# Optimization experiments

Measured on AMD Instinct MI355X. Metric: run time of the kernel, lower is better.

## Reference

```python
import jax, jax.numpy as jnp
import numpy as np

SPP_SIZES = (1, 3, 6, 8)  # -> 1+9+36+64 = 110 pooled tokens


def conv1x1(x, w, b):
    # x: [B,C,H,W], w: [O,C], b: [O] -> [B,O,H,W]
    return jnp.einsum('bchw,oc->bohw', x, w) + b[None, :, None, None]


def spp(t):
    # t: [B,C,H,W] with H,W divisible by every size -> [B,C,110]
    B, C, H, W = t.shape
    outs = []
    for s in SPP_SIZES:
        p = t.reshape(B, C, s, H // s, s, W // s).mean(axis=(3, 5))
        outs.append(p.reshape(B, C, s * s))
    return jnp.concatenate(outs, axis=-1)


def setup_inputs() -> dict:
    key = jax.random.key(0)
    ks = jax.random.split(key, 9)
    B, C, H, W = 8, 512, 96, 96
    inner = 256
    sc = 1.0 / np.sqrt(C)
    return {
        'x': jax.random.normal(ks[0], (B, C, H, W), dtype=jnp.float32),
        'phi_w': jax.random.normal(ks[1], (inner, C), dtype=jnp.float32) * sc,
        'phi_b': jnp.zeros((inner,), dtype=jnp.float32),
        'theta_w': jax.random.normal(ks[2], (inner, C), dtype=jnp.float32) * sc,
        'theta_b': jnp.zeros((inner,), dtype=jnp.float32),
        'gamma_w': jax.random.normal(ks[3], (inner, C), dtype=jnp.float32) * sc,
        'gamma_b': jnp.zeros((inner,), dtype=jnp.float32),
        'W_w': jax.random.normal(ks[4], (C, inner), dtype=jnp.float32) * (1.0 / np.sqrt(inner)),
        'W_b': jnp.zeros((C,), dtype=jnp.float32),
    }


def reference(x, phi_w, phi_b, theta_w, theta_b, gamma_w, gamma_b, W_w, W_b):
    B, C, H, W = x.shape
    HW = H * W
    phi = jax.nn.relu(conv1x1(x, phi_w, phi_b))      # [B,256,H,W]
    theta = jax.nn.relu(conv1x1(x, theta_w, theta_b))
    gamma = conv1x1(x, gamma_w, gamma_b)
    theta_p = spp(theta)                              # [B,256,110]
    gamma_p = spp(gamma)                              # [B,256,110]
    # Faithful to original: raw reshape (NOT a transpose) of [B,256,H,W] -> [B,HW,256]
    phi_r = jnp.reshape(phi, (B, HW, 256))
    y1 = jnp.einsum('bnc,bck->bnk', phi_r, theta_p)   # [B,HW,110]
    y1_norm = jax.nn.softmax(y1 * (HW ** -0.25), axis=-1)
    y2 = jnp.einsum('bnk,bkc->bnc', y1_norm, jnp.transpose(gamma_p, (0, 2, 1)))  # [B,HW,256]
    # Faithful raw reshape back to [B,256,H,W]
    y2_r = jnp.reshape(y2, (B, 256, H, W))
    y2_w = conv1x1(y2_r, W_w, W_b)                    # [B,C,H,W]
    return x + y2_w
```

## Files before the change

### kernel.cpp

```cpp
#include <hip/hip_runtime.h>

#define NB 8
#define CIN 512
#define OIN 256
#define HWN 9216
#define KP 110
#define SCL 0.10206207261596577f

typedef __attribute__((ext_vector_type(8))) short bf16x8;
typedef __attribute__((ext_vector_type(4))) float f32x4;
typedef unsigned short u16;

__device__ inline unsigned bf16_1(float a) {
    unsigned u = __builtin_bit_cast(unsigned, a);
    return (u + 0x7fffu + ((u >> 16) & 1u)) >> 16;
}
__device__ inline unsigned bf16_pack(float a, float b) {
    return bf16_1(a) | (bf16_1(b) << 16);
}
__device__ inline float b2f(u16 u) {
    return __builtin_bit_cast(float, ((unsigned)u) << 16);
}

__device__ __forceinline__ void gload16(const u16* g, u16* l) {
    __builtin_amdgcn_global_load_lds(
        (const __attribute__((address_space(1))) unsigned int*)g,
        (__attribute__((address_space(3))) unsigned int*)l, 16, 0, 0);
}

__global__ __launch_bounds__(256) void castw_kernel(
    const float* __restrict__ phi_w, const float* __restrict__ theta_w,
    const float* __restrict__ Ww,
    u16* __restrict__ Wcat, u16* __restrict__ Wwb)
{
    int i = blockIdx.x * 256 + threadIdx.x;
    if (i < 262144) {
        float v = (i < 131072) ? phi_w[i] : theta_w[i - 131072];
        Wcat[i] = (u16)bf16_1(v);
    } else {
        int j = i - 262144;
        Wwb[j] = (u16)bf16_1(Ww[j]);
    }
}

__global__ __launch_bounds__(256) void castx_kernel(
    const float* __restrict__ x, u16* __restrict__ xT)
{
    const int t = threadIdx.x;
    const int tx = t & 15, ty = t >> 4;
    const int b = blockIdx.z;
    const int c0 = blockIdx.y * 64;
    const int hw0 = blockIdx.x * 64;

    const float* xb = x + ((size_t)b * CIN + c0 + ty * 4) * HWN + hw0 + tx * 4;
    float4 v[4];
#pragma unroll
    for (int q = 0; q < 4; ++q)
        v[q] = *(const float4*)(xb + (size_t)q * HWN);

    u16* dst = xT + ((size_t)b * HWN + hw0 + tx * 4) * CIN + c0 + ty * 4;
    const float* f = (const float*)v;
#pragma unroll
    for (int p = 0; p < 4; ++p) {
        uint2 o = {bf16_pack(f[0 * 4 + p], f[1 * 4 + p]),
                   bf16_pack(f[2 * 4 + p], f[3 * 4 + p])};
        *(uint2*)(dst + (size_t)p * CIN) = o;
    }
}

template<int KDIM, int MODE>
__global__ __launch_bounds__(256, 4) void gemm_kernel(
    const u16* __restrict__ A,
    const u16* __restrict__ Bw,
    const float* __restrict__ b0, const float* __restrict__ b1,
    const float* __restrict__ resid,
    void* __restrict__ out0_, void* __restrict__ out1_)
{
    __shared__ u16 As[2][128 * 32];
    __shared__ u16 Bs[2][128 * 32];

    constexpr int NSTEP = KDIM / 32;
    constexpr int NWG = 72 * 4 * NB;

    const int id = blockIdx.x;
    const int swz = (id & 7) * (NWG / 8) + (id >> 3);
    const int u = swz % 288;
    const int bz = swz / 288;
    const int by = u & 3;
    const int bx = u >> 2;

    const int t = threadIdx.x;
    const int m0 = bx * 128;
    const int n0 = by * 128;
    const int w = t >> 6, l = t & 63;
    const int wr = w >> 1, wc = w & 1;
    const int g = l >> 4, li = l & 15;

    const u16* Ab = A + (size_t)bz * HWN * KDIM + (size_t)m0 * KDIM;
    const u16* Bb = Bw + (size_t)n0 * KDIM;

    f32x4 zero = {0.f, 0.f, 0.f, 0.f};
    f32x4 acc[4][4];
#pragma unroll
    for (int i = 0; i < 4; ++i)
#pragma unroll
        for (int j = 0; j < 4; ++j) acc[i][j] = zero;

    auto stage = [&](int step, int buf) {
#pragma unroll
        for (int j = 0; j < 2; ++j) {
            int c = j * 256 + t;
            int row = c >> 2, slot = c & 3;
            int ss = slot ^ ((row >> 1) & 3);
            gload16(Ab + (size_t)row * KDIM + step * 32 + ss * 8, &As[buf][c * 8]);
        }
#pragma unroll
        for (int j = 0; j < 2; ++j) {
            int c = j * 256 + t;
            int row = c >> 2, slot = c & 3;
            int ss = slot ^ ((row >> 1) & 3);
            gload16(Bb + (size_t)row * KDIM + step * 32 + ss * 8, &Bs[buf][c * 8]);
        }
    };

    stage(0, 0);
    asm volatile("s_waitcnt vmcnt(0)" ::: "memory");
    __builtin_amdgcn_s_barrier();

    int cur = 0;
#pragma unroll 1
    for (int s = 0; s < NSTEP; ++s) {
        if (s + 1 < NSTEP) stage(s + 1, cur ^ 1);

        bf16x8 af[4], bv[4];
#pragma unroll
        for (int mi = 0; mi < 4; ++mi) {
            int r = wr * 64 + mi * 16 + li;
            int sl = g ^ ((r >> 1) & 3);
            af[mi] = *(const bf16x8*)&As[cur][r * 32 + sl * 8];
        }
#pragma unroll
        for (int ni = 0; ni < 4; ++ni) {
            int r = wc * 64 + ni * 16 + li;
            int sl = g ^ ((r >> 1) & 3);
            bv[ni] = *(const bf16x8*)&Bs[cur][r * 32 + sl * 8];
        }
#pragma unroll
        for (int mi = 0; mi < 4; ++mi)
#pragma unroll
            for (int ni = 0; ni < 4; ++ni)
                acc[mi][ni] = __builtin_amdgcn_mfma_f32_16x16x32_bf16(
                    af[mi], bv[ni], acc[mi][ni], 0, 0, 0);

        if (s + 1 < NSTEP) {
            asm volatile("s_waitcnt vmcnt(0)" ::: "memory");
            __builtin_amdgcn_s_barrier();
            cur ^= 1;
        }
    }

#pragma unroll
    for (int ni = 0; ni < 4; ++ni) {
        int n = n0 + wc * 64 + ni * 16 + li;
        if constexpr (MODE == 0) {
            float bias = (n < 256) ? b0[n] : b1[n - 256];
            u16* dst = (u16*)((n < 256) ? out0_ : out1_) + ((size_t)bz * 256 + (n & 255)) * HWN;
#pragma unroll
            for (int mi = 0; mi < 4; ++mi) {
                int m = m0 + wr * 64 + mi * 16 + (g << 2);
                f32x4 v = acc[mi][ni];
                float e0 = fmaxf(v.x + bias, 0.f), e1 = fmaxf(v.y + bias, 0.f);
                float e2 = fmaxf(v.z + bias, 0.f), e3 = fmaxf(v.w + bias, 0.f);
                uint2 pk = {bf16_pack(e0, e1), bf16_pack(e2, e3)};
                *(uint2*)(dst + m) = pk;
            }
        } else {
            float bias = b0[n];
            float* dst = (float*)out0_ + ((size_t)bz * 512 + n) * HWN;
            const float* res = resid + ((size_t)bz * 512 + n) * HWN;
#pragma unroll
            for (int mi = 0; mi < 4; ++mi) {
                int m = m0 + wr * 64 + mi * 16 + (g << 2);
                f32x4 v = acc[mi][ni];
                float4 rx = *(const float4*)(res + m);
                float4 o = {v.x + bias + rx.x, v.y + bias + rx.y,
                            v.z + bias + rx.z, v.w + bias + rx.w};
                *(float4*)(dst + m) = o;
            }
        }
    }
}

__global__ __launch_bounds__(256) void pool_x_kernel(
    const float* __restrict__ in, float* __restrict__ out)
{
    __shared__ float ps[576];
    const int plane = blockIdx.x;
    const float* p = in + (size_t)plane * HWN;
    const int t = threadIdx.x;

    for (int i = t; i < 576; i += 256) {
        int bh = i / 24, bw = i % 24;
        float s = 0.f;
#pragma unroll
        for (int r = 0; r < 4; ++r) {
            float4 v = *(const float4*)&p[(bh * 4 + r) * 96 + bw * 4];
            s += v.x + v.y + v.z + v.w;
        }
        ps[i] = s;
    }
    __syncthreads();

    if (t < KP) {
        float s = 0.f;
        if (t == 0) {
            for (int i = 0; i < 576; ++i) s += ps[i];
            s *= (1.0f / 9216.0f);
        } else if (t < 10) {
            int idx = t - 1, bi = idx / 3, bj = idx % 3;
            for (int r = 0; r < 8; ++r)
                for (int c = 0; c < 8; ++c)
                    s += ps[(bi * 8 + r) * 24 + bj * 8 + c];
            s *= (1.0f / 1024.0f);
        } else if (t < 46) {
            int idx = t - 10, bi = idx / 6, bj = idx % 6;
            for (int r = 0; r < 4; ++r)
                for (int c = 0; c < 4; ++c)
                    s += ps[(bi * 4 + r) * 24 + bj * 4 + c];
            s *= (1.0f / 256.0f);
        } else {
            int idx = t - 46, bi = idx / 8, bj = idx % 8;
            for (int r = 0; r < 3; ++r)
                for (int c = 0; c < 3; ++c)
                    s += ps[(bi * 3 + r) * 24 + bj * 3 + c];
            s *= (1.0f / 144.0f);
        }
        out[(size_t)plane * KP + t] = s;
    }
}

__global__ __launch_bounds__(256) void pool_t_kernel(
    const u16* __restrict__ in, u16* __restrict__ outT)
{
    __shared__ float ps[576];
    const int plane = blockIdx.x;
    const int b = plane >> 8, c = plane & 255;
    const u16* p = in + (size_t)plane * HWN;
    const int t = threadIdx.x;

    for (int i = t; i < 576; i += 256) {
        int bh = i / 24, bw = i % 24;
        float s = 0.f;
#pragma unroll
        for (int r = 0; r < 4; ++r) {
            ushort4 v = *(const ushort4*)&p[(bh * 4 + r) * 96 + bw * 4];
            s += b2f(v.x) + b2f(v.y) + b2f(v.z) + b2f(v.w);
        }
        ps[i] = s;
    }
    __syncthreads();

    if (t < 128) {
        float s = 0.f;
        if (t == 0) {
            for (int i = 0; i < 576; ++i) s += ps[i];
            s *= (1.0f / 9216.0f);
        } else if (t < 10) {
            int idx = t - 1, bi = idx / 3, bj = idx % 3;
            for (int r = 0; r < 8; ++r)
                for (int cc = 0; cc < 8; ++cc)
                    s += ps[(bi * 8 + r) * 24 + bj * 8 + cc];
            s *= (1.0f / 1024.0f);
        } else if (t < 46) {
            int idx = t - 10, bi = idx / 6, bj = idx % 6;
            for (int r = 0; r < 4; ++r)
                for (int cc = 0; cc < 4; ++cc)
                    s += ps[(bi * 4 + r) * 24 + bj * 4 + cc];
            s *= (1.0f / 256.0f);
        } else if (t < KP) {
            int idx = t - 46, bi = idx / 8, bj = idx % 8;
            for (int r = 0; r < 3; ++r)
                for (int cc = 0; cc < 3; ++cc)
                    s += ps[(bi * 3 + r) * 24 + bj * 3 + cc];
            s *= (1.0f / 144.0f);
        } else {
            s = 0.f;
        }
        outT[((size_t)b * 128 + t) * 256 + c] = (u16)bf16_1(s);
    }
}

__global__ __launch_bounds__(256) void gammap_kernel(
    const float* __restrict__ xp,
    const float* __restrict__ gw,
    const float* __restrict__ gb,
    u16* __restrict__ gp)
{
    const int k = blockIdx.x, b = blockIdx.y;
    const int t = threadIdx.x;
    if (k >= KP) {
        gp[((size_t)b * 256 + t) * 128 + k] = 0;
        return;
    }
    __shared__ float xc[512];
    xc[t]       = xp[((size_t)b * CIN + t) * KP + k];
    xc[t + 256] = xp[((size_t)b * CIN + t + 256) * KP + k];
    __syncthreads();

    float acc = gb[t];
    const float* wrow = gw + (size_t)t * CIN;
#pragma unroll 4
    for (int c = 0; c < CIN; c += 4) {
        float4 wv = *(const float4*)&wrow[c];
        acc = fmaf(wv.x, xc[c], acc);
        acc = fmaf(wv.y, xc[c + 1], acc);
        acc = fmaf(wv.z, xc[c + 2], acc);
        acc = fmaf(wv.w, xc[c + 3], acc);
    }
    gp[((size_t)b * 256 + t) * 128 + k] = (u16)bf16_1(acc);
}

__global__ __launch_bounds__(256) void attn_kernel(
    const u16* __restrict__ phi,
    const u16* __restrict__ tpT,
    const u16* __restrict__ gp,
    u16* __restrict__ y2T)
{
    __shared__ __align__(16) u16 smem[32768];
    u16* As = smem;
    u16* Bs = smem + 8192;
    char* Pb = (char*)(smem + 16384);

    const int t = threadIdx.x;
    const int w = t >> 6, l = t & 63;
    const int g = l >> 4, li = l & 15;
    const int b = blockIdx.y;
    const int rr = blockIdx.x >> 1;
    const int ci0 = (blockIdx.x & 1) << 7;

    const u16* phib = phi + (size_t)b * (OIN * HWN);
    const u16* tpb  = tpT + (size_t)b * (128 * 256);
    const u16* gpb  = gp  + (size_t)b * (256 * 128);

    const int srow = t >> 3;
    const int su = t & 7;

    f32x4 zero = {0.f, 0.f, 0.f, 0.f};
    f32x4 acc[2][8];
#pragma unroll
    for (int i = 0; i < 2; ++i)
#pragma unroll
        for (int j = 0; j < 8; ++j) acc[i][j] = zero;

    for (int kt = 0; kt < 256; kt += 64) {
#pragma unroll
        for (int cc = 0; cc < 4; ++cc) {
            int row = cc * 32 + srow;
            int ss = su ^ (row & 7);
            gload16(phib + (size_t)(ci0 + row) * HWN + rr * 256 + kt + ss * 8,
                    &As[(row * 8 + su) * 8]);
        }
#pragma unroll
        for (int cc = 0; cc < 4; ++cc) {
            int row = cc * 32 + srow;
            int ss = su ^ (row & 7);
            gload16(tpb + (size_t)row * 256 + kt + ss * 8,
                    &Bs[(row * 8 + su) * 8]);
        }
        __syncthreads();

#pragma unroll
        for (int h = 0; h < 2; ++h) {
            bf16x8 af[2], bfr[8];
#pragma unroll
            for (int mi = 0; mi < 2; ++mi) {
                int r = w * 32 + mi * 16 + li;
                af[mi] = *(const bf16x8*)&As[r * 64 + (((h * 4 + g) ^ (r & 7)) << 3)];
            }
#pragma unroll
            for (int ni = 0; ni < 8; ++ni) {
                int r = ni * 16 + li;
                bfr[ni] = *(const bf16x8*)&Bs[r * 64 + (((h * 4 + g) ^ (r & 7)) << 3)];
            }
#pragma unroll
            for (int mi = 0; mi < 2; ++mi)
#pragma unroll
                for (int ni = 0; ni < 8; ++ni)
                    acc[mi][ni] = __builtin_amdgcn_mfma_f32_16x16x32_bf16(
                        af[mi], bfr[ni], acc[mi][ni], 0, 0, 0);
        }
        __syncthreads();
    }

    bool vm[8];
#pragma unroll
    for (int ni = 0; ni < 8; ++ni) vm[ni] = (ni * 16 + li) < KP;

#pragma unroll
    for (int mi = 0; mi < 2; ++mi) {
#pragma unroll
        for (int r = 0; r < 4; ++r) {
            float mx = -1e30f;
#pragma unroll
            for (int ni = 0; ni < 8; ++ni)
                if (vm[ni]) mx = fmaxf(mx, acc[mi][ni][r] * SCL);
            mx = fmaxf(mx, __shfl_xor(mx, 1));
            mx = fmaxf(mx, __shfl_xor(mx, 2));
            mx = fmaxf(mx, __shfl_xor(mx, 4));
            mx = fmaxf(mx, __shfl_xor(mx, 8));
            float s = 0.f;
#pragma unroll
            for (int ni = 0; ni < 8; ++ni) {
                float e = vm[ni] ? __expf(acc[mi][ni][r] * SCL - mx) : 0.f;
                acc[mi][ni][r] = e;
                s += e;
            }
            s += __shfl_xor(s, 1);
            s += __shfl_xor(s, 2);
            s += __shfl_xor(s, 4);
            s += __shfl_xor(s, 8);
            float inv = 1.0f / s;
#pragma unroll
            for (int ni = 0; ni < 8; ++ni) acc[mi][ni][r] *= inv;
        }
#pragma unroll
        for (int ni = 0; ni < 8; ++ni)
#pragma unroll
            for (int r = 0; r < 4; ++r) {
                int row = w * 32 + mi * 16 + g * 4 + r;
                int col = ni * 16 + li;
                *(short*)(Pb + row * 256 + (((col >> 3) ^ (row & 7)) << 4) + ((col & 7) << 1)) =
                    (short)bf16_1(acc[mi][ni][r]);
            }
    }

    f32x4 acc2[2][16];
#pragma unroll
    for (int i = 0; i < 2; ++i)
#pragma unroll
        for (int j = 0; j < 16; ++j) acc2[i][j] = zero;

#pragma unroll 1
    for (int ks2 = 0; ks2 < 2; ++ks2) {
#pragma unroll
        for (int cc = 0; cc < 8; ++cc) {
            int row = cc * 32 + srow;
            int ss = su ^ (row & 7);
            gload16(gpb + (size_t)row * 128 + ks2 * 64 + ss * 8,
                    &smem[(row * 8 + su) * 8]);
        }
        __syncthreads();

#pragma unroll
        for (int h = 0; h < 2; ++h) {
            bf16x8 a2[2];
#pragma unroll
            for (int mi = 0; mi < 2; ++mi) {
                int prow = w * 32 + mi * 16 + li;
                int s = ks2 * 8 + h * 4 + g;
                a2[mi] = *(const bf16x8*)(Pb + prow * 256 + ((s ^ (prow & 7)) << 4));
            }
#pragma unroll
            for (int cf = 0; cf < 16; ++cf) {
                int crow = cf * 16 + li;
                bf16x8 bv = *(const bf16x8*)&smem[crow * 64 + (((h * 4 + g) ^ (crow & 7)) << 3)];
#pragma unroll
                for (int mi = 0; mi < 2; ++mi)
                    acc2[mi][cf] = __builtin_amdgcn_mfma_f32_16x16x32_bf16(
                        a2[mi], bv, acc2[mi][cf], 0, 0, 0);
            }
        }
        __syncthreads();
    }

#pragma unroll
    for (int mi = 0; mi < 2; ++mi)
#pragma unroll
        for (int cf = 0; cf < 16; ++cf) {
            int c = cf * 16 + li;
            int cib = w * 32 + mi * 16 + g * 4;
            int e0 = c * 128 + (cib ^ (li << 3));
            unsigned d0 = bf16_pack(acc2[mi][cf][0], acc2[mi][cf][1]);
            unsigned d1 = bf16_pack(acc2[mi][cf][2], acc2[mi][cf][3]);
            *(unsigned*)((char*)smem + (size_t)e0 * 2) = d0;
            *(unsigned*)((char*)smem + (size_t)e0 * 2 + 4) = d1;
        }

    __syncthreads();

    {
        u16* yb = y2T + ((size_t)b * HWN + rr * 256) * 256 + ci0;
#pragma unroll
        for (int j = 0; j < 16; ++j) {
            int c = (t >> 4) + (j << 4);
            int e = c * 128 + (((t & 15) ^ (t >> 4)) << 3);
            uint4 v = *(const uint4*)((char*)smem + (size_t)e * 2);
            *(uint4*)(yb + (size_t)c * 256 + (t & 15) * 8) = v;
        }
    }
}

extern "C" void kernel_launch(void* const* d_in, const int* in_sizes, int n_in,
                              void* d_out, int out_size, void* d_ws, size_t ws_size,
                              hipStream_t stream)
{
    const float* x       = (const float*)d_in[0];
    const float* phi_w   = (const float*)d_in[1];
    const float* phi_b   = (const float*)d_in[2];
    const float* theta_w = (const float*)d_in[3];
    const float* theta_b = (const float*)d_in[4];
    const float* gamma_w = (const float*)d_in[5];
    const float* gamma_b = (const float*)d_in[6];
    const float* W_w     = (const float*)d_in[7];
    const float* W_b     = (const float*)d_in[8];
    float* out = (float*)d_out;

    char* p = (char*)d_ws;
    u16* xT     = (u16*)p;  p += (size_t)NB * HWN * CIN * 2;
    u16* phi_bf = (u16*)p;  p += (size_t)NB * OIN * HWN * 2;
    u16* th_y2  = (u16*)p;  p += (size_t)NB * OIN * HWN * 2;
    float* xp   = (float*)p; p += (size_t)NB * CIN * KP * 4;
    u16* tpT    = (u16*)p;  p += (size_t)NB * 128 * 256 * 2;
    u16* gp     = (u16*)p;  p += (size_t)NB * 256 * 128 * 2;
    u16* Wcat   = (u16*)p;  p += 512 * 512 * 2;
    u16* Wwb    = (u16*)p;  p += 512 * 256 * 2;

    castw_kernel<<<1536, 256, 0, stream>>>(phi_w, theta_w, W_w, Wcat, Wwb);
    castx_kernel<<<dim3(144, 8, NB), 256, 0, stream>>>(x, xT);
    gemm_kernel<512, 0><<<dim3(72 * 4 * NB), 256, 0, stream>>>(
        xT, Wcat, phi_b, theta_b, nullptr, phi_bf, th_y2);
    pool_x_kernel<<<dim3(NB * CIN), 256, 0, stream>>>(x, xp);
    pool_t_kernel<<<dim3(NB * OIN), 256, 0, stream>>>(th_y2, tpT);
    gammap_kernel<<<dim3(128, NB), 256, 0, stream>>>(xp, gamma_w, gamma_b, gp);
    attn_kernel<<<dim3(72, NB), 256, 0, stream>>>(phi_bf, tpT, gp, th_y2);
    gemm_kernel<256, 1><<<dim3(72 * 4 * NB), 256, 0, stream>>>(
        th_y2, Wwb, W_b, nullptr, x, out, nullptr);
}
```

Measured before the change: 349.0 us.

## Split attention tiles finer, batch gamma projection over eight pooled tokens

The attention kernel now has each block handle 64 phi channels instead of 128. This doubles the grid to 144x8, shrinks per-wave accumulators, and sets launch bounds for 4 blocks per CU, all to raise occupancy. The gamma GEMV kernel computes 8 pooled positions per block from a shared tile, cutting redundant weight reads and block count. pool_x is moved ahead of the main GEMM launch. The cost is that theta-pool tiles are reloaded twice as often, and the second GEMM is re-staged in 32-wide chunks with more barriers.

New measurement: 307.5 us. 11.9% less time.

```diff
diff --git a/kernel.cpp b/kernel.cpp
--- a/kernel.cpp
+++ b/kernel.cpp
@@ -296,47 +296,65 @@
     const float* __restrict__ gb,
     u16* __restrict__ gp)
 {
-    const int k = blockIdx.x, b = blockIdx.y;
+    __shared__ float xc[8][512];
+    const int kb = blockIdx.x * 8, b = blockIdx.y;
     const int t = threadIdx.x;
-    if (k >= KP) {
-        gp[((size_t)b * 256 + t) * 128 + k] = 0;
-        return;
-    }
-    __shared__ float xc[512];
-    xc[t]       = xp[((size_t)b * CIN + t) * KP + k];
-    xc[t + 256] = xp[((size_t)b * CIN + t + 256) * KP + k];
+
+#pragma unroll
+    for (int j = 0; j < 16; ++j) {
+        int idx = j * 256 + t;
+        int kk = idx >> 9, c = idx & 511;
+        int k = kb + kk;
+        xc[kk][c] = (k < KP) ? xp[((size_t)b * CIN + c) * KP + k] : 0.f;
+    }
     __syncthreads();
 
-    float acc = gb[t];
+    float bias = gb[t];
+    float acc[8];
+#pragma unroll
+    for (int kk = 0; kk < 8; ++kk) acc[kk] = bias;
+
     const float* wrow = gw + (size_t)t * CIN;
-#pragma unroll 4
+#pragma unroll 2
     for (int c = 0; c < CIN; c += 4) {
         float4 wv = *(const float4*)&wrow[c];
-        acc = fmaf(wv.x, xc[c], acc);
-        acc = fmaf(wv.y, xc[c + 1], acc);
-        acc = fmaf(wv.z, xc[c + 2], acc);
-        acc = fmaf(wv.w, xc[c + 3], acc);
-    }
-    gp[((size_t)b * 256 + t) * 128 + k] = (u16)bf16_1(acc);
-}
-
-__global__ __launch_bounds__(256) void attn_kernel(
+#pragma unroll
+        for (int kk = 0; kk < 8; ++kk) {
+            acc[kk] = fmaf(wv.x, xc[kk][c], acc[kk]);
+            acc[kk] = fmaf(wv.y, xc[kk][c + 1], acc[kk]);
+            acc[kk] = fmaf(wv.z, xc[kk][c + 2], acc[kk]);
+            acc[kk] = fmaf(wv.w, xc[kk][c + 3], acc[kk]);
+        }
+    }
+
+    ushort4 o0, o1;
+    o0.x = (u16)bf16_1(acc[0]); o0.y = (u16)bf16_1(acc[1]);
+    o0.z = (u16)bf16_1(acc[2]); o0.w = (u16)bf16_1(acc[3]);
+    o1.x = (u16)bf16_1(acc[4]); o1.y = (u16)bf16_1(acc[5]);
+    o1.z = (u16)bf16_1(acc[6]); o1.w = (u16)bf16_1(acc[7]);
+    u16* dst = gp + ((size_t)b * 256 + t) * 128 + kb;
+    *(ushort4*)(dst) = o0;
+    *(ushort4*)(dst + 4) = o1;
+}
+
+__global__ __launch_bounds__(256, 4) void attn_kernel(
     const u16* __restrict__ phi,
     const u16* __restrict__ tpT,
     const u16* __restrict__ gp,
     u16* __restrict__ y2T)
 {
-    __shared__ __align__(16) u16 smem[32768];
-    u16* As = smem;
-    u16* Bs = smem + 8192;
-    char* Pb = (char*)(smem + 16384);
+    __shared__ __align__(16) char smem[40960];
+    u16* As = (u16*)smem;
+    u16* Bs = (u16*)(smem + 8192);
+    char* Pb = smem + 24576;
+    u16* Gs = (u16*)smem;
 
     const int t = threadIdx.x;
     const int w = t >> 6, l = t & 63;
     const int g = l >> 4, li = l & 15;
     const int b = blockIdx.y;
-    const int rr = blockIdx.x >> 1;
-    const int ci0 = (blockIdx.x & 1) << 7;
+    const int rr = blockIdx.x >> 2;
+    const int ci0 = (blockIdx.x & 3) << 6;
 
     const u16* phib = phi + (size_t)b * (OIN * HWN);
     const u16* tpb  = tpT + (size_t)b * (128 * 256);
@@ -346,15 +364,13 @@
     const int su = t & 7;
 
     f32x4 zero = {0.f, 0.f, 0.f, 0.f};
-    f32x4 acc[2][8];
-#pragma unroll
-    for (int i = 0; i < 2; ++i)
-#pragma unroll
-        for (int j = 0; j < 8; ++j) acc[i][j] = zero;
+    f32x4 acc[8];
+#pragma unroll
+    for (int j = 0; j < 8; ++j) acc[j] = zero;
 
     for (int kt = 0; kt < 256; kt += 64) {
 #pragma unroll
-        for (int cc = 0; cc < 4; ++cc) {
+        for (int cc = 0; cc < 2; ++cc) {
             int row = cc * 32 + srow;
             int ss = su ^ (row & 7);
             gload16(phib + (size_t)(ci0 + row) * HWN + rr * 256 + kt + ss * 8,
@@ -371,23 +387,18 @@
 
 #pragma unroll
         for (int h = 0; h < 2; ++h) {
-            bf16x8 af[2], bfr[8];
-#pragma unroll
-            for (int mi = 0; mi < 2; ++mi) {
-                int r = w * 32 + mi * 16 + li;
-                af[mi] = *(const bf16x8*)&As[r * 64 + (((h * 4 + g) ^ (r & 7)) << 3)];
+            int r = w * 16 + li;
+            bf16x8 af = *(const bf16x8*)&As[r * 64 + (((h * 4 + g) ^ (r & 7)) << 3)];
+            bf16x8 bfr[8];
+#pragma unroll
+            for (int ni = 0; ni < 8; ++ni) {
+                int rb = ni * 16 + li;
+                bfr[ni] = *(const bf16x8*)&Bs[rb * 64 + (((h * 4 + g) ^ (rb & 7)) << 3)];
             }
 #pragma unroll
-            for (int ni = 0; ni < 8; ++ni) {
-                int r = ni * 16 + li;
-                bfr[ni] = *(const bf16x8*)&Bs[r * 64 + (((h * 4 + g) ^ (r & 7)) << 3)];
-            }
-#pragma unroll
-            for (int mi = 0; mi < 2; ++mi)
-#pragma unroll
-                for (int ni = 0; ni < 8; ++ni)
-                    acc[mi][ni] = __builtin_amdgcn_mfma_f32_16x16x32_bf16(
-                        af[mi], bfr[ni], acc[mi][ni], 0, 0, 0);
+            for (int ni = 0; ni < 8; ++ni)
+                acc[ni] = __builtin_amdgcn_mfma_f32_16x16x32_bf16(
+                    af, bfr[ni], acc[ni], 0, 0, 0);
         }
         __syncthreads();
     }
@@ -397,105 +408,87 @@
     for (int ni = 0; ni < 8; ++ni) vm[ni] = (ni * 16 + li) < KP;
 
 #pragma unroll
-    for (int mi = 0; mi < 2; ++mi) {
+    for (int r = 0; r < 4; ++r) {
+        float mx = -1e30f;
+#pragma unroll
+        for (int ni = 0; ni < 8; ++ni)
+            if (vm[ni]) mx = fmaxf(mx, acc[ni][r] * SCL);
+        mx = fmaxf(mx, __shfl_xor(mx, 1));
+        mx = fmaxf(mx, __shfl_xor(mx, 2));
+        mx = fmaxf(mx, __shfl_xor(mx, 4));
+        mx = fmaxf(mx, __shfl_xor(mx, 8));
+        float s = 0.f;
+#pragma unroll
+        for (int ni = 0; ni < 8; ++ni) {
+            float e = vm[ni] ? __expf(acc[ni][r] * SCL - mx) : 0.f;
+            acc[ni][r] = e;
+            s += e;
+        }
+        s += __shfl_xor(s, 1);
+        s += __shfl_xor(s, 2);
+        s += __shfl_xor(s, 4);
+        s += __shfl_xor(s, 8);
+        float inv = 1.0f / s;
+#pragma unroll
+        for (int ni = 0; ni < 8; ++ni) acc[ni][r] *= inv;
+    }
+#pragma unroll
+    for (int ni = 0; ni < 8; ++ni)
 #pragma unroll
         for (int r = 0; r < 4; ++r) {
-            float mx = -1e30f;
-#pragma unroll
-            for (int ni = 0; ni < 8; ++ni)
-                if (vm[ni]) mx = fmaxf(mx, acc[mi][ni][r] * SCL);
-            mx = fmaxf(mx, __shfl_xor(mx, 1));
-            mx = fmaxf(mx, __shfl_xor(mx, 2));
-            mx = fmaxf(mx, __shfl_xor(mx, 4));
-            mx = fmaxf(mx, __shfl_xor(mx, 8));
-            float s = 0.f;
-#pragma unroll
-            for (int ni = 0; ni < 8; ++ni) {
-                float e = vm[ni] ? __expf(acc[mi][ni][r] * SCL - mx) : 0.f;
-                acc[mi][ni][r] = e;
-                s += e;
-            }
-            s += __shfl_xor(s, 1);
-            s += __shfl_xor(s, 2);
-            s += __shfl_xor(s, 4);
-            s += __shfl_xor(s, 8);
-            float inv = 1.0f / s;
-#pragma unroll
-            for (int ni = 0; ni < 8; ++ni) acc[mi][ni][r] *= inv;
-        }
-#pragma unroll
-        for (int ni = 0; ni < 8; ++ni)
-#pragma unroll
-            for (int r = 0; r < 4; ++r) {
-                int row = w * 32 + mi * 16 + g * 4 + r;
-                int col = ni * 16 + li;
-                *(short*)(Pb + row * 256 + (((col >> 3) ^ (row & 7)) << 4) + ((col & 7) << 1)) =
-                    (short)bf16_1(acc[mi][ni][r]);
-            }
-    }
-
-    f32x4 acc2[2][16];
-#pragma unroll
-    for (int i = 0; i < 2; ++i)
-#pragma unroll
-        for (int j = 0; j < 16; ++j) acc2[i][j] = zero;
+            int row = w * 16 + g * 4 + r;
+            int col = ni * 16 + li;
+            *(short*)(Pb + row * 256 + (((col >> 3) ^ (row & 7)) << 4) + ((col & 7) << 1)) =
+                (short)bf16_1(acc[ni][r]);
+        }
+
+    f32x4 acc2[16];
+#pragma unroll
+    for (int j = 0; j < 16; ++j) acc2[j] = zero;
 
 #pragma unroll 1
-    for (int ks2 = 0; ks2 < 2; ++ks2) {
-#pragma unroll
-        for (int cc = 0; cc < 8; ++cc) {
-            int row = cc * 32 + srow;
-            int ss = su ^ (row & 7);
-            gload16(gpb + (size_t)row * 128 + ks2 * 64 + ss * 8,
-                    &smem[(row * 8 + su) * 8]);
+    for (int ch = 0; ch < 4; ++ch) {
+#pragma unroll
+        for (int j = 0; j < 4; ++j) {
+            int row = j * 64 + (t >> 2);
+            int slot = t & 3;
+            int ss = slot ^ (row & 3);
+            gload16(gpb + (size_t)row * 128 + ch * 32 + ss * 8,
+                    &Gs[(j * 256 + t) * 8]);
         }
         __syncthreads();
 
-#pragma unroll
-        for (int h = 0; h < 2; ++h) {
-            bf16x8 a2[2];
-#pragma unroll
-            for (int mi = 0; mi < 2; ++mi) {
-                int prow = w * 32 + mi * 16 + li;
-                int s = ks2 * 8 + h * 4 + g;
-                a2[mi] = *(const bf16x8*)(Pb + prow * 256 + ((s ^ (prow & 7)) << 4));
-            }
-#pragma unroll
-            for (int cf = 0; cf < 16; ++cf) {
-                int crow = cf * 16 + li;
-                bf16x8 bv = *(const bf16x8*)&smem[crow * 64 + (((h * 4 + g) ^ (crow & 7)) << 3)];
-#pragma unroll
-                for (int mi = 0; mi < 2; ++mi)
-                    acc2[mi][cf] = __builtin_amdgcn_mfma_f32_16x16x32_bf16(
-                        a2[mi], bv, acc2[mi][cf], 0, 0, 0);
-            }
+        int prow = w * 16 + li;
+        bf16x8 a2 = *(const bf16x8*)(Pb + prow * 256 + (((ch * 4 + g) ^ (prow & 7)) << 4));
+#pragma unroll
+        for (int cf = 0; cf < 16; ++cf) {
+            int crow = cf * 16 + li;
+            bf16x8 bv = *(const bf16x8*)((const char*)Gs + crow * 64 + ((g ^ (crow & 3)) << 4));
+            acc2[cf] = __builtin_amdgcn_mfma_f32_16x16x32_bf16(a2, bv, acc2[cf], 0, 0, 0);
         }
         __syncthreads();
     }
 
 #pragma unroll
-    for (int mi = 0; mi < 2; ++mi)
-#pragma unroll
-        for (int cf = 0; cf < 16; ++cf) {
-            int c = cf * 16 + li;
-            int cib = w * 32 + mi * 16 + g * 4;
-            int e0 = c * 128 + (cib ^ (li << 3));
-            unsigned d0 = bf16_pack(acc2[mi][cf][0], acc2[mi][cf][1]);
-            unsigned d1 = bf16_pack(acc2[mi][cf][2], acc2[mi][cf][3]);
-            *(unsigned*)((char*)smem + (size_t)e0 * 2) = d0;
-            *(unsigned*)((char*)smem + (size_t)e0 * 2 + 4) = d1;
-        }
+    for (int cf = 0; cf < 16; ++cf) {
+        int c = cf * 16 + li;
+        int cib = w * 16 + g * 4;
+        int e0 = c * 64 + (cib ^ ((li & 7) << 3));
+        unsigned d0 = bf16_pack(acc2[cf][0], acc2[cf][1]);
+        unsigned d1 = bf16_pack(acc2[cf][2], acc2[cf][3]);
+        *(unsigned*)(smem + (size_t)e0 * 2) = d0;
+        *(unsigned*)(smem + (size_t)e0 * 2 + 4) = d1;
+    }
 
     __syncthreads();
 
     {
-        u16* yb = y2T + ((size_t)b * HWN + rr * 256) * 256 + ci0;
-#pragma unroll
-        for (int j = 0; j < 16; ++j) {
-            int c = (t >> 4) + (j << 4);
-            int e = c * 128 + (((t & 15) ^ (t >> 4)) << 3);
-            uint4 v = *(const uint4*)((char*)smem + (size_t)e * 2);
-            *(uint4*)(yb + (size_t)c * 256 + (t & 15) * 8) = v;
+        int c = t;
+        u16* dst = y2T + ((size_t)b * HWN + rr * 256 + c) * 256 + ci0;
+#pragma unroll
+        for (int j = 0; j < 8; ++j) {
+            uint4 v = *(const uint4*)(smem + c * 128 + ((j ^ (c & 7)) << 4));
+            *(uint4*)(dst + j * 8) = v;
         }
     }
 }
@@ -527,12 +520,12 @@
 
     castw_kernel<<<1536, 256, 0, stream>>>(phi_w, theta_w, W_w, Wcat, Wwb);
     castx_kernel<<<dim3(144, 8, NB), 256, 0, stream>>>(x, xT);
+    pool_x_kernel<<<dim3(NB * CIN), 256, 0, stream>>>(x, xp);
     gemm_kernel<512, 0><<<dim3(72 * 4 * NB), 256, 0, stream>>>(
         xT, Wcat, phi_b, theta_b, nullptr, phi_bf, th_y2);
-    pool_x_kernel<<<dim3(NB * CIN), 256, 0, stream>>>(x, xp);
     pool_t_kernel<<<dim3(NB * OIN), 256, 0, stream>>>(th_y2, tpT);
-    gammap_kernel<<<dim3(128, NB), 256, 0, stream>>>(xp, gamma_w, gamma_b, gp);
-    attn_kernel<<<dim3(72, NB), 256, 0, stream>>>(phi_bf, tpT, gp, th_y2);
+    gammap_kernel<<<dim3(16, NB), 256, 0, stream>>>(xp, gamma_w, gamma_b, gp);
+    attn_kernel<<<dim3(144, NB), 256, 0, stream>>>(phi_bf, tpT, gp, th_y2);
     gemm_kernel<256, 1><<<dim3(72 * 4 * NB), 256, 0, stream>>>(
         th_y2, Wwb, W_b, nullptr, x, out, nullptr);
 }
```
